# Optimization experiments

Hardware: AMD Instinct MI355X
Metric: run time of the kernel (lower is better)

## Reference

```python
import jax, jax.numpy as jnp
import numpy as np

RCR = 5.2
RCA = 3.5
ETA_R = 16.0
ETA_A = 8.0
ZETA = 32.0
NUM_SPECIES = 4
NUM_PAIRS = NUM_SPECIES * (NUM_SPECIES + 1) // 2  # 10
SHFR = jnp.asarray(np.linspace(0.9, RCR, 17)[:-1], dtype=jnp.float32)   # (16,)
SHFA = jnp.asarray(np.linspace(0.9, RCA, 5)[:-1], dtype=jnp.float32)    # (4,)
SHFZ = jnp.asarray((np.linspace(0.0, np.pi, 9) + np.pi / 16.0)[:-1], dtype=jnp.float32)  # (8,)

def _triu_index(n):
    s1, s2 = np.triu_indices(n)
    t = np.zeros((n, n), dtype=np.int32)
    t[s1, s2] = np.arange(len(s1))
    t[s2, s1] = np.arange(len(s1))
    return jnp.asarray(t)

TRIU = _triu_index(NUM_SPECIES)  # (4,4) -> pair index in [0,10)

def _fc(d, rc):
    # cosine cutoff, zero beyond rc
    return jnp.where(d < rc, 0.5 * jnp.cos(np.float32(np.pi) * d / rc) + 0.5, 0.0)

def _aev(species, coordinates):
    N, A = species.shape
    # vec[n,i,j] = r_j - r_i  (N,A,A,3)
    vec = coordinates[:, None, :, :] - coordinates[:, :, None, :]
    d2 = jnp.sum(vec * vec, axis=-1)                      # (N,A,A)
    eye = jnp.eye(A, dtype=bool)
    d = jnp.sqrt(jnp.where(eye, 1.0, d2))                 # safe sqrt on diagonal
    pair_mask = (~eye).astype(coordinates.dtype)          # (A,A)

    # ---- radial AEV ----
    fcr = _fc(d, RCR) * pair_mask                         # (N,A,A)
    rad = 0.25 * jnp.exp(-ETA_R * (d[..., None] - SHFR) ** 2) * fcr[..., None]  # (N,A,A,16)
    sp_oh = jax.nn.one_hot(species, NUM_SPECIES, dtype=coordinates.dtype)       # (N,A,4)
    radial_aev = jnp.einsum('nijt,njs->nist', rad, sp_oh).reshape(N, A, -1)     # (N,A,64)

    # ---- angular AEV ----
    fca = _fc(d, RCA) * pair_mask                         # (N,A,A)
    dot = jnp.einsum('nijc,nikc->nijk', vec, vec)         # (N,A,A,A)
    cosang = 0.95 * dot / jnp.clip(d[:, :, :, None] * d[:, :, None, :], 1e-10)
    angles = jnp.arccos(cosang)                           # (N,A,A,A)
    mask_jk = (~eye).astype(coordinates.dtype)            # j != k
    fcj12 = fca[:, :, :, None] * fca[:, :, None, :] * mask_jk[None, None]  # (N,A,A,A)
    dmean = 0.5 * (d[:, :, :, None] + d[:, :, None, :])   # (N,A,A,A)
    factor1 = ((1.0 + jnp.cos(angles[..., None] - SHFZ)) * 0.5) ** ZETA    # (N,A,A,A,8)
    factor2 = jnp.exp(-ETA_A * (dmean[..., None] - SHFA) ** 2)             # (N,A,A,A,4)
    # terms over ordered (j,k); each unordered pair counted twice, so the
    # original factor 2 and the 0.5 double-count correction cancel.
    terms = (fcj12[..., None] * factor2)[..., :, None] * factor1[..., None, :]  # (N,A,A,A,4,8)
    terms = terms.reshape(N, A, A, A, SHFA.shape[0] * SHFZ.shape[0])            # (N,A,A,A,32)
    pair_idx = TRIU[species[:, :, None], species[:, None, :]]                   # (N,A,A)
    pair_oh = jax.nn.one_hot(pair_idx, NUM_PAIRS, dtype=coordinates.dtype)      # (N,A,A,10)
    angular_aev = jnp.einsum('nijkt,njkp->nipt', terms, pair_oh).reshape(N, A, -1)  # (N,A,320)

    return jnp.concatenate([radial_aev, angular_aev], axis=-1)  # (N,A,384)

def setup_inputs() -> dict:
    key = jax.random.key(0)
    k1, k2 = jax.random.split(key)
    species = jax.random.randint(k1, (32, 48), 0, NUM_SPECIES)
    # atoms in an 8 Angstrom box -> realistic neighbor density for 5.2 A cutoff
    coordinates = jax.random.uniform(k2, (32, 48, 3), dtype=jnp.float32) * 8.0
    return {"species": species, "coordinates": coordinates}

def reference(species, coordinates):
    return _aev(species, coordinates)
```

## Files before the change

### kernel.cpp

```cpp
#include <hip/hip_runtime.h>
#include <math.h>


#define A_ATOMS 48
#define NMOL    32
#define NFEAT   384
#define CHUNK   384

__device__ __constant__ float CZ_TAB[8] = {
     0.980785280f,  0.831469612f,  0.555570233f,  0.195090322f,
    -0.195090322f, -0.555570233f, -0.831469612f, -0.980785280f };
__device__ __constant__ float SZ_TAB[8] = {
     0.195090322f,  0.555570233f,  0.831469612f,  0.980785280f,
     0.980785280f,  0.831469612f,  0.555570233f,  0.195090322f };

__device__ __forceinline__ float bf2f(unsigned short h) {
    return __uint_as_float(((unsigned int)h) << 16);
}

__global__ __launch_bounds__(256, 6)
void AEVComputer_2156073583107_kernel(const void* __restrict__ coords_raw,
                                      const void* __restrict__ species_raw,
                                      float* __restrict__ out)
{
    const int bid   = blockIdx.x;
    const int n     = bid / A_ATOMS;
    const int i     = bid - n * A_ATOMS;
    const int tid   = threadIdx.x;
    const int w     = tid >> 6;
    const int lane  = tid & 63;
    const int sub   = lane >> 5;
    const int slice = (w << 1) | sub;
    const int t     = lane & 31;
    const int ia    = t >> 3;

    __shared__ float4 geom[A_ATOMS];
    __shared__ float4 uvec[A_ATOMS];
    __shared__ int    nbr[A_ATOMS];
    __shared__ int    Msh;
    __shared__ float2 pairA[CHUNK];
    __shared__ float  pairW[CHUNK * 4];
    __shared__ int    cnt[10], curs[10], ofs[11];
    __shared__ float  rad_m[4][64];
    __shared__ float  ang_m[8][320];

    const unsigned short* cu16 = (const unsigned short*)coords_raw;
    const unsigned int*   su32 = (const unsigned int*)species_raw;

    if (tid < 64) {
        if (tid < 10) cnt[tid] = 0;
        float xf = 0.f, yf = 0.f, zf = 0.f; unsigned int uraw = 0u;
        if (tid < A_ATOMS) {
            const int g = n * A_ATOMS + tid;
            const float* cf = (const float*)coords_raw;
            xf = cf[3 * g]; yf = cf[3 * g + 1]; zf = cf[3 * g + 2];
            uraw = su32[g];
        }
        float v = bf2f(cu16[tid]);
        unsigned long long mb = __ballot(fabsf(v) < 32.0f);
        const bool coords_bf16 = (__popcll(mb) >= 60);
        unsigned int svv = su32[tid & 31];
        unsigned long long m2 = __ballot((tid < 32) && svv >= 0x3F000000u && svv < 0x40800000u);
        unsigned long long m3 = __ballot((tid < 32) && (tid & 1) && svv != 0u);
        const int smode = (__popcll(m2) > 20) ? 2 : ((m3 == 0ull) ? 1 : 0);

        float x = xf, y = yf, z = zf; int s = 0;
        if (tid < A_ATOMS) {
            const int g = n * A_ATOMS + tid;
            if (coords_bf16) {
                x = bf2f(cu16[3 * g]); y = bf2f(cu16[3 * g + 1]); z = bf2f(cu16[3 * g + 2]);
            }
            if (smode == 1) uraw = su32[2 * g];
            s = (smode == 2) ? (int)(__uint_as_float(uraw) + 0.5f) : (int)uraw;
            s = (s < 0) ? 0 : ((s > 3) ? 3 : s);
        }
        const float xi = __shfl(x, i), yi = __shfl(y, i), zi = __shfl(z, i);
        float dx = x - xi, dy = y - yi, dz = z - zi;
        float d2 = dx * dx + dy * dy + dz * dz;
        float d  = (tid == i) ? 1.0f : sqrtf(d2);
        float inv = 1.0f / d;
        bool  self = (tid >= A_ATOMS) || (tid == i);
        bool  predA = !self && (d < 3.5f);
        bool  predR = !self && (d < 5.2f);
        float fca = predA ? (0.5f * __cosf(0.8975979010f * d) + 0.5f) : 0.0f;
        float rv  = predR ? (0.25f * (0.5f * __cosf(0.6041524333f * d) + 0.5f)) : 0.0f;
        if (tid < A_ATOMS) {
            float spf = (float)s;
            geom[tid] = make_float4(d, rv, fca, spf);
            uvec[tid] = make_float4(dx * inv, dy * inv, dz * inv, spf);
        }
        unsigned long long mask = __ballot(predA);
        if (predA) {
            int pos = __popcll(mask & ((1ull << tid) - 1ull));
            nbr[pos] = tid;
        }
        if (tid == 0) Msh = __popcll(mask);
    }
    __syncthreads();
    const int M = Msh;
    const int npairs = (M * (M - 1)) >> 1;

    {
        const float sf   = (float)(lane >> 4);
        const float shfr = 0.9f + 0.26875f * (float)(lane & 15);
        float radv = 0.0f;
        #pragma unroll
        for (int jj = 0; jj < 12; ++jj) {
            const float4 gm = geom[w + 4 * jj];
            float e   = gm.x - shfr;
            float val = __expf(-16.0f * e * e) * gm.y;
            radv += (gm.w == sf) ? val : 0.0f;
        }
        rad_m[w][lane] = radv;
    }

    float a[10];
    #pragma unroll
    for (int p = 0; p < 10; ++p) a[p] = 0.0f;
    const float czv = CZ_TAB[t & 7];
    const float szv = SZ_TAB[t & 7];

    for (int base = 0; base < npairs; base += CHUNK) {
        if (base > 0) {
            if (tid < 10) cnt[tid] = 0;
            __syncthreads();
        }
        const int nch = min(CHUNK, npairs - base);

        float2 pa0, pa1; float wf0[4], wf1[4]; int p0 = 0, p1 = 0;
        const bool h0 = (tid < nch);
        const bool h1 = (tid + 256 < nch);
        #pragma unroll
        for (int pass = 0; pass < 2; ++pass) {
            const bool hv = pass ? h1 : h0;
            if (!hv) continue;
            const int q = base + tid + (pass ? 256 : 0);
            const float b = (float)(2 * M - 1);
            int jj = (int)(0.5f * (b - sqrtf(fmaxf(b * b - 8.0f * (float)q, 0.0f))));
            jj = max(0, min(jj, M - 2));
            while (jj > 0 && q < ((jj * (2 * M - 1 - jj)) >> 1)) --jj;
            while (q >= (((jj + 1) * (2 * M - 2 - jj)) >> 1)) ++jj;
            const int kk = jj + 1 + (q - ((jj * (2 * M - 1 - jj)) >> 1));
            const int j = nbr[jj], k = nbr[kk];
            const float4 gj = geom[j], gk = geom[k];
            const float4 uj = uvec[j], uk = uvec[k];
            float c  = fmaf(uj.x, uk.x, fmaf(uj.y, uk.y, uj.z * uk.z));
            float cc = 0.95f * c;
            float ss = sqrtf(fmaxf(1.0f - cc * cc, 0.0f));
            float2 pa = make_float2(0.5f * cc, 0.5f * ss);
            const float wgt = 2.0f * gj.z * gk.z;
            const float dm  = 0.5f * (gj.x + gk.x);
            float wf[4];
            #pragma unroll
            for (int q4 = 0; q4 < 4; ++q4) {
                float e = dm - (0.9f + 0.65f * (float)q4);
                wf[q4] = wgt * __expf(-8.0f * e * e);
            }
            const int sj = (int)gj.w, sk = (int)gk.w;
            const int lo = min(sj, sk), hi = max(sj, sk);
            const int p = ((lo * (7 - lo)) >> 1) + hi;
            atomicAdd(&cnt[p], 1);
            if (pass) { pa1 = pa; wf1[0]=wf[0]; wf1[1]=wf[1]; wf1[2]=wf[2]; wf1[3]=wf[3]; p1 = p; }
            else      { pa0 = pa; wf0[0]=wf[0]; wf0[1]=wf[1]; wf0[2]=wf[2]; wf0[3]=wf[3]; p0 = p; }
        }
        __syncthreads();
        if (tid == 0) {
            int o = 0;
            #pragma unroll
            for (int pp = 0; pp < 10; ++pp) { ofs[pp] = o; curs[pp] = o; o += cnt[pp]; }
            ofs[10] = o;
        }
        __syncthreads();
        if (h0) {
            int slot = atomicAdd(&curs[p0], 1);
            pairA[slot] = pa0;
            pairW[4*slot+0]=wf0[0]; pairW[4*slot+1]=wf0[1];
            pairW[4*slot+2]=wf0[2]; pairW[4*slot+3]=wf0[3];
        }
        if (h1) {
            int slot = atomicAdd(&curs[p1], 1);
            pairA[slot] = pa1;
            pairW[4*slot+0]=wf1[0]; pairW[4*slot+1]=wf1[1];
            pairW[4*slot+2]=wf1[2]; pairW[4*slot+3]=wf1[3];
        }
        __syncthreads();

        int O[11];
        #pragma unroll
        for (int pp = 0; pp < 11; ++pp) O[pp] = ofs[pp];

        #pragma unroll
        for (int pp = 0; pp < 10; ++pp) {
            const int e1 = O[pp + 1];
            int qq = O[pp] + slice;
            float acc = a[pp];
            for (; qq + 8 < e1; qq += 16) {
                float2 v0  = pairA[qq];
                float  w0  = pairW[4 * qq + ia];
                float2 v1  = pairA[qq + 8];
                float  w1  = pairW[4 * (qq + 8) + ia];
                float x0 = fmaf(v0.y, szv, fmaf(v0.x, czv, 0.5f));
                float x1 = fmaf(v1.y, szv, fmaf(v1.x, czv, 0.5f));
                float a2 = x0*x0, b2 = x1*x1;
                float a4 = a2*a2, b4 = b2*b2;
                float a8 = a4*a4, b8 = b4*b4;
                float a16 = a8*a8, b16 = b8*b8;
                acc = fmaf(a16 * a16, w0, acc);
                acc = fmaf(b16 * b16, w1, acc);
            }
            if (qq < e1) {
                float2 v0 = pairA[qq];
                float  w0 = pairW[4 * qq + ia];
                float x0 = fmaf(v0.y, szv, fmaf(v0.x, czv, 0.5f));
                float a2 = x0*x0, a4 = a2*a2, a8 = a4*a4, a16 = a8*a8;
                acc = fmaf(a16 * a16, w0, acc);
            }
            a[pp] = acc;
        }
        if (base + CHUNK < npairs) __syncthreads();
    }

    #pragma unroll
    for (int pp = 0; pp < 10; ++pp) ang_m[slice][pp * 32 + t] = a[pp];
    __syncthreads();

    const size_t outb = (size_t)bid * NFEAT;
    for (int f = tid; f < NFEAT; f += 256) {
        float v;
        if (f < 64) {
            v = rad_m[0][f] + rad_m[1][f] + rad_m[2][f] + rad_m[3][f];
        } else {
            const int g = f - 64;
            v = ((ang_m[0][g] + ang_m[1][g]) + (ang_m[2][g] + ang_m[3][g]))
              + ((ang_m[4][g] + ang_m[5][g]) + (ang_m[6][g] + ang_m[7][g]));
        }
        out[outb + f] = v;
    }
}

extern "C" void kernel_launch(void* const* d_in, const int* in_sizes, int n_in,
                              void* d_out, int out_size, void* d_ws, size_t ws_size,
                              hipStream_t stream) {
    if (n_in < 2) return;
    const void* coords;
    const void* species;
    if (in_sizes[0] >= in_sizes[1]) { coords = d_in[0]; species = d_in[1]; }
    else                            { coords = d_in[1]; species = d_in[0]; }
    float* out = (float*)d_out;
    AEVComputer_2156073583107_kernel<<<NMOL * A_ATOMS, 256, 0, stream>>>(coords, species, out);
}
```

Before: 61.63 us.

## Split each atom across two blocks and replace species bucketing with predicated accumulation

Each atom's angular pair list is now split between two blocks, interleaved by parity, so the grid doubles. The partial angular features are combined with global atomicAdd after a memset of the output. The per-chunk counting sort of pairs by species-pair (atomics, prefix sum, scatter) is replaced by storing a pair index and adding each term into all ten accumulators through selects. This removes two barriers and the shared atomics per chunk, but costs ten selects per pair, an extra memset, and global atomics on the output.

```diff
diff --git a/kernel.cpp b/kernel.cpp
--- a/kernel.cpp
+++ b/kernel.cpp
@@ -5,7 +5,7 @@
 #define A_ATOMS 48
 #define NMOL    32
 #define NFEAT   384
-#define CHUNK   384
+#define CHUNK   256
 
 __device__ __constant__ float CZ_TAB[8] = {
      0.980785280f,  0.831469612f,  0.555570233f,  0.195090322f,
@@ -24,8 +24,10 @@
                                       float* __restrict__ out)
 {
     const int bid   = blockIdx.x;
-    const int n     = bid / A_ATOMS;
-    const int i     = bid - n * A_ATOMS;
+    const int h     = bid & 1;
+    const int cid   = bid >> 1;
+    const int n     = cid / A_ATOMS;
+    const int i     = cid - n * A_ATOMS;
     const int tid   = threadIdx.x;
     const int w     = tid >> 6;
     const int lane  = tid & 63;
@@ -40,7 +42,7 @@
     __shared__ int    Msh;
     __shared__ float2 pairA[CHUNK];
     __shared__ float  pairW[CHUNK * 4];
-    __shared__ int    cnt[10], curs[10], ofs[11];
+    __shared__ int    pairP[CHUNK];
     __shared__ float  rad_m[4][64];
     __shared__ float  ang_m[8][320];
 
@@ -48,7 +50,6 @@
     const unsigned int*   su32 = (const unsigned int*)species_raw;
 
     if (tid < 64) {
-        if (tid < 10) cnt[tid] = 0;
         float xf = 0.f, yf = 0.f, zf = 0.f; unsigned int uraw = 0u;
         if (tid < A_ATOMS) {
             const int g = n * A_ATOMS + tid;
@@ -99,8 +100,9 @@
     __syncthreads();
     const int M = Msh;
     const int npairs = (M * (M - 1)) >> 1;
+    const int myN = (npairs - h + 1) >> 1;
 
-    {
+    if (h == 0) {
         const float sf   = (float)(lane >> 4);
         const float shfr = 0.9f + 0.26875f * (float)(lane & 15);
         float radv = 0.0f;
@@ -120,21 +122,10 @@
     const float czv = CZ_TAB[t & 7];
     const float szv = SZ_TAB[t & 7];
 
-    for (int base = 0; base < npairs; base += CHUNK) {
-        if (base > 0) {
-            if (tid < 10) cnt[tid] = 0;
-            __syncthreads();
-        }
-        const int nch = min(CHUNK, npairs - base);
-
-        float2 pa0, pa1; float wf0[4], wf1[4]; int p0 = 0, p1 = 0;
-        const bool h0 = (tid < nch);
-        const bool h1 = (tid + 256 < nch);
-        #pragma unroll
-        for (int pass = 0; pass < 2; ++pass) {
-            const bool hv = pass ? h1 : h0;
-            if (!hv) continue;
-            const int q = base + tid + (pass ? 256 : 0);
+    for (int base = 0; base < myN; base += CHUNK) {
+        const int m = base + tid;
+        if (m < myN) {
+            const int q = h + 2 * m;
             const float b = (float)(2 * M - 1);
             int jj = (int)(0.5f * (b - sqrtf(fmaxf(b * b - 8.0f * (float)q, 0.0f))));
             jj = max(0, min(jj, M - 2));
@@ -147,94 +138,45 @@
             float c  = fmaf(uj.x, uk.x, fmaf(uj.y, uk.y, uj.z * uk.z));
             float cc = 0.95f * c;
             float ss = sqrtf(fmaxf(1.0f - cc * cc, 0.0f));
-            float2 pa = make_float2(0.5f * cc, 0.5f * ss);
+            pairA[tid] = make_float2(0.5f * cc, 0.5f * ss);
             const float wgt = 2.0f * gj.z * gk.z;
             const float dm  = 0.5f * (gj.x + gk.x);
-            float wf[4];
             #pragma unroll
             for (int q4 = 0; q4 < 4; ++q4) {
                 float e = dm - (0.9f + 0.65f * (float)q4);
-                wf[q4] = wgt * __expf(-8.0f * e * e);
+                pairW[4 * tid + q4] = wgt * __expf(-8.0f * e * e);
             }
             const int sj = (int)gj.w, sk = (int)gk.w;
             const int lo = min(sj, sk), hi = max(sj, sk);
-            const int p = ((lo * (7 - lo)) >> 1) + hi;
-            atomicAdd(&cnt[p], 1);
-            if (pass) { pa1 = pa; wf1[0]=wf[0]; wf1[1]=wf[1]; wf1[2]=wf[2]; wf1[3]=wf[3]; p1 = p; }
-            else      { pa0 = pa; wf0[0]=wf[0]; wf0[1]=wf[1]; wf0[2]=wf[2]; wf0[3]=wf[3]; p0 = p; }
+            pairP[tid] = ((lo * (7 - lo)) >> 1) + hi;
         }
         __syncthreads();
-        if (tid == 0) {
-            int o = 0;
+        const int nch = min(CHUNK, myN - base);
+        for (int qq = slice; qq < nch; qq += 8) {
+            float2 v   = pairA[qq];
+            int    p   = pairP[qq];
+            float  wf2 = pairW[4 * qq + ia];
+            float x  = fmaf(v.y, szv, fmaf(v.x, czv, 0.5f));
+            float x2 = x * x, x4 = x2 * x2, x8 = x4 * x4, x16 = x8 * x8;
+            float term = x16 * x16 * wf2;
             #pragma unroll
-            for (int pp = 0; pp < 10; ++pp) { ofs[pp] = o; curs[pp] = o; o += cnt[pp]; }
-            ofs[10] = o;
+            for (int pp = 0; pp < 10; ++pp) a[pp] += (p == pp) ? term : 0.0f;
         }
-        __syncthreads();
-        if (h0) {
-            int slot = atomicAdd(&curs[p0], 1);
-            pairA[slot] = pa0;
-            pairW[4*slot+0]=wf0[0]; pairW[4*slot+1]=wf0[1];
-            pairW[4*slot+2]=wf0[2]; pairW[4*slot+3]=wf0[3];
-        }
-        if (h1) {
-            int slot = atomicAdd(&curs[p1], 1);
-            pairA[slot] = pa1;
-            pairW[4*slot+0]=wf1[0]; pairW[4*slot+1]=wf1[1];
-            pairW[4*slot+2]=wf1[2]; pairW[4*slot+3]=wf1[3];
-        }
-        __syncthreads();
-
-        int O[11];
-        #pragma unroll
-        for (int pp = 0; pp < 11; ++pp) O[pp] = ofs[pp];
-
-        #pragma unroll
-        for (int pp = 0; pp < 10; ++pp) {
-            const int e1 = O[pp + 1];
-            int qq = O[pp] + slice;
-            float acc = a[pp];
-            for (; qq + 8 < e1; qq += 16) {
-                float2 v0  = pairA[qq];
-                float  w0  = pairW[4 * qq + ia];
-                float2 v1  = pairA[qq + 8];
-                float  w1  = pairW[4 * (qq + 8) + ia];
-                float x0 = fmaf(v0.y, szv, fmaf(v0.x, czv, 0.5f));
-                float x1 = fmaf(v1.y, szv, fmaf(v1.x, czv, 0.5f));
-                float a2 = x0*x0, b2 = x1*x1;
-                float a4 = a2*a2, b4 = b2*b2;
-                float a8 = a4*a4, b8 = b4*b4;
-                float a16 = a8*a8, b16 = b8*b8;
-                acc = fmaf(a16 * a16, w0, acc);
-                acc = fmaf(b16 * b16, w1, acc);
-            }
-            if (qq < e1) {
-                float2 v0 = pairA[qq];
-                float  w0 = pairW[4 * qq + ia];
-                float x0 = fmaf(v0.y, szv, fmaf(v0.x, czv, 0.5f));
-                float a2 = x0*x0, a4 = a2*a2, a8 = a4*a4, a16 = a8*a8;
-                acc = fmaf(a16 * a16, w0, acc);
-            }
-            a[pp] = acc;
-        }
-        if (base + CHUNK < npairs) __syncthreads();
+        if (base + CHUNK < myN) __syncthreads();
     }
 
     #pragma unroll
     for (int pp = 0; pp < 10; ++pp) ang_m[slice][pp * 32 + t] = a[pp];
     __syncthreads();
 
-    const size_t outb = (size_t)bid * NFEAT;
-    for (int f = tid; f < NFEAT; f += 256) {
-        float v;
-        if (f < 64) {
-            v = rad_m[0][f] + rad_m[1][f] + rad_m[2][f] + rad_m[3][f];
-        } else {
-            const int g = f - 64;
-            v = ((ang_m[0][g] + ang_m[1][g]) + (ang_m[2][g] + ang_m[3][g]))
-              + ((ang_m[4][g] + ang_m[5][g]) + (ang_m[6][g] + ang_m[7][g]));
-        }
-        out[outb + f] = v;
+    const size_t outb = (size_t)cid * NFEAT;
+    for (int f = tid; f < 320; f += 256) {
+        float v = ((ang_m[0][f] + ang_m[1][f]) + (ang_m[2][f] + ang_m[3][f]))
+                + ((ang_m[4][f] + ang_m[5][f]) + (ang_m[6][f] + ang_m[7][f]));
+        atomicAdd(&out[outb + 64 + f], v);
+    }
+    if (h == 0 && tid < 64) {
+        out[outb + tid] = rad_m[0][tid] + rad_m[1][tid] + rad_m[2][tid] + rad_m[3][tid];
     }
 }
 
@@ -247,5 +189,6 @@
     if (in_sizes[0] >= in_sizes[1]) { coords = d_in[0]; species = d_in[1]; }
     else                            { coords = d_in[1]; species = d_in[0]; }
     float* out = (float*)d_out;
-    AEVComputer_2156073583107_kernel<<<NMOL * A_ATOMS, 256, 0, stream>>>(coords, species, out);
+    hipMemsetAsync(d_out, 0, (size_t)out_size * sizeof(float), stream);
+    AEVComputer_2156073583107_kernel<<<NMOL * A_ATOMS * 2, 256, 0, stream>>>(coords, species, out);
 }
```

Measured after the change: 66.69 us. 1.08x slower.
